# Optimization experiments

Hardware: AMD Instinct MI355X
Metric: run time of the kernel (lower is better)

Reference implementation:

```python
import jax, jax.numpy as jnp
import numpy as np

N_CLASSES = 1000
N_CENTERS = 4
SIGMA = 10.0
HIDDEN = 512
BATCH = 512


def setup_inputs() -> dict:
    key = jax.random.key(0)
    k1, k2 = jax.random.split(key)
    f = jax.random.normal(k1, (BATCH, HIDDEN), dtype=jnp.float32)
    # he_normal: std = sqrt(2 / fan_in), fan_in = hidden
    W = jax.random.normal(k2, (N_CLASSES, N_CENTERS, HIDDEN), dtype=jnp.float32) * np.sqrt(2.0 / HIDDEN)
    return {"f": f, "W": W}


def reference(f, W):
    n_classes, n_centers, hidden = W.shape
    mc = n_classes * n_centers
    w_flat = W.reshape(mc, hidden)  # [mc, h]

    # squared euclidean distance f<->centers via ||f||^2 + ||w||^2 - 2 f.w
    f_sq = jnp.sum(f * f, axis=-1, keepdims=True)            # [b, 1]
    w_sq = jnp.sum(w_flat * w_flat, axis=-1)                 # [mc]
    fw = jnp.einsum('bh,mh->bm', f, w_flat)                  # [b, mc]
    fw_norm = (f_sq + w_sq[None, :] - 2.0 * fw).reshape(f.shape[0], n_classes, n_centers)
    distance = jnp.max(jnp.exp(-fw_norm / SIGMA), axis=-1)   # [b, n_classes]

    # pairwise center distances, strict upper triangle regularizer
    ww = jnp.einsum('mh,nh->mn', w_flat, w_flat)             # [mc, mc]
    w_norm_mat = w_sq[:, None] + w_sq[None, :] - 2.0 * ww
    upper_mask = jnp.triu(jnp.ones((mc, mc), dtype=f.dtype), k=1)
    w_norm_upper = w_norm_mat * upper_mask
    denom = 2.0 / (mc * mc - mc)
    mu = denom * jnp.sum(w_norm_upper)
    residuals = ((w_norm_upper - mu) ** 2) * upper_mask
    rw = denom * jnp.sum(residuals)

    rw_col = jnp.full((f.shape[0], 1), rw, dtype=f.dtype) * jnp.ones((1, 1), dtype=f.dtype)
    rw_col = jnp.ones((f.shape[0], 1), dtype=f.dtype) * rw
    return jnp.concatenate([distance, rw_col], axis=-1)      # [b, n_classes+1]
```

## Files before the change

kernel.cpp:

```cpp
#include <hip/hip_runtime.h>


#define HIDDEN  512
#define BATCH   512
#define NCLASS  1000
#define MC      4000
#define MCPAD   4096
#define OUTW    1001
#define PAIRS   7998000.0

typedef __attribute__((ext_vector_type(8))) short bf16x8;
typedef __attribute__((ext_vector_type(4))) float f32x4;

static __device__ __forceinline__ unsigned short bfr(float x) {
  unsigned u = __float_as_uint(x);
  u += 0x7FFF + ((u >> 16) & 1);
  return (unsigned short)(u >> 16);
}
static __device__ __forceinline__ unsigned int pack2bf(float a, float b) {
  unsigned ua = __float_as_uint(a); ua += 0x7FFF + ((ua >> 16) & 1);
  unsigned ub = __float_as_uint(b); ub += 0x7FFF + ((ub >> 16) & 1);
  return (ua >> 16) | (ub & 0xFFFF0000u);
}

template <int STEPS>
static __device__ __forceinline__ void gemm22(
    const unsigned short* __restrict__ aP0, const unsigned short* __restrict__ aP1,
    const unsigned short* __restrict__ bP0, const unsigned short* __restrict__ bP1,
    f32x4 acc[2][2]) {
  bf16x8 aC[2], bC[2];
  aC[0] = *(const bf16x8*)aP0; aC[1] = *(const bf16x8*)aP1;
  bC[0] = *(const bf16x8*)bP0; bC[1] = *(const bf16x8*)bP1;
  #pragma unroll
  for (int kb = 0; kb < STEPS; kb++) {
    bf16x8 aN[2], bN[2];
    if (kb < STEPS - 1) {
      int off = (kb + 1) * 32;
      aN[0] = *(const bf16x8*)(aP0 + off); aN[1] = *(const bf16x8*)(aP1 + off);
      bN[0] = *(const bf16x8*)(bP0 + off); bN[1] = *(const bf16x8*)(bP1 + off);
    }
    #pragma unroll
    for (int mi = 0; mi < 2; mi++)
      #pragma unroll
      for (int ni = 0; ni < 2; ni++)
        acc[mi][ni] = __builtin_amdgcn_mfma_f32_16x16x32_bf16(aC[mi], bC[ni], acc[mi][ni], 0, 0, 0);
    if (kb < STEPS - 1) {
      aC[0] = aN[0]; aC[1] = aN[1]; bC[0] = bN[0]; bC[1] = bN[1];
    }
  }
}

__global__ __launch_bounds__(256) void prep_all_kernel(
    const float* __restrict__ f, const float* __restrict__ w,
    unsigned short* __restrict__ w2, unsigned short* __restrict__ f2,
    unsigned short* __restrict__ wt,
    float* __restrict__ w_sq, float* __restrict__ f_sq,
    float* __restrict__ s) {
  int bid = blockIdx.x;
  int t = threadIdx.x;
  if (bid < 1152) {
    if (bid == 0) { s[t] = 0.0f; s[t + 256] = 0.0f; }
    int lane = t & 63, wid = t >> 6;
    int row = bid * 4 + wid;
    const float* src = nullptr;
    unsigned short* dst2;
    float* dstsq;
    bool pad = false;
    if (row < MCPAD) {
      if (row < MC) src = w + (size_t)row * HIDDEN; else pad = true;
      dst2 = w2 + (size_t)row * HIDDEN; dstsq = w_sq + row;
    } else {
      int fr = row - MCPAD;
      src = f + (size_t)fr * HIDDEN;
      dst2 = f2 + (size_t)fr * HIDDEN; dstsq = f_sq + fr;
    }
    float4 a = {0.f,0.f,0.f,0.f}, b = {0.f,0.f,0.f,0.f};
    if (!pad) {
      const float4* s4 = (const float4*)src;
      a = s4[2 * lane]; b = s4[2 * lane + 1];
    }
    float sq = a.x*a.x + a.y*a.y + a.z*a.z + a.w*a.w
             + b.x*b.x + b.y*b.y + b.z*b.z + b.w*b.w;
    #pragma unroll
    for (int off = 32; off >= 1; off >>= 1) sq += __shfl_down(sq, off);
    if (lane == 0) *dstsq = sq;
    uint4 p;
    p.x = pack2bf(a.x, a.y); p.y = pack2bf(a.z, a.w);
    p.z = pack2bf(b.x, b.y); p.w = pack2bf(b.z, b.w);
    ((uint4*)dst2)[lane] = p;
  } else {
    int b2 = bid - 1152;
    int kb = b2 >> 3, ab = b2 & 7;
    __shared__ unsigned short tile[64][72];
    int c4 = (t & 15) * 4, r0 = t >> 4;
    #pragma unroll
    for (int i = 0; i < 4; i++) {
      int r = r0 + i * 16;
      int gk = kb * 64 + r;
      float4 v = {0.f,0.f,0.f,0.f};
      if (gk < MC) v = *(const float4*)&w[(size_t)gk * HIDDEN + ab * 64 + c4];
      tile[c4 + 0][r] = bfr(v.x);
      tile[c4 + 1][r] = bfr(v.y);
      tile[c4 + 2][r] = bfr(v.z);
      tile[c4 + 3][r] = bfr(v.w);
    }
    __syncthreads();
    #pragma unroll
    for (int i = 0; i < 4; i++) {
      int a = r0 + i * 16;
      uint2 v = *(const uint2*)&tile[a][c4];
      *(uint2*)&wt[(size_t)(ab * 64 + a) * MCPAD + kb * 64 + c4] = v;
    }
  }
}

__global__ __launch_bounds__(256) void colsum_kernel(
    const float* __restrict__ w, float* __restrict__ s) {
  int c = threadIdx.x * 2;
  int r0 = blockIdx.x * 125;
  float a0 = 0.f, a1 = 0.f;
  #pragma unroll 5
  for (int r = 0; r < 125; r++) {
    float2 v = *(const float2*)&w[(size_t)(r0 + r) * HIDDEN + c];
    a0 += v.x; a1 += v.y;
  }
  atomicAdd(&s[c], a0);
  atomicAdd(&s[c + 1], a1);
}

__global__ __launch_bounds__(256, 2) void main_kernel(
    const float* __restrict__ wOrig,
    const unsigned short* __restrict__ f2, const unsigned short* __restrict__ w2,
    const unsigned short* __restrict__ wt,
    const float* __restrict__ w_sq, const float* __restrict__ f_sq,
    const float* __restrict__ s,
    float* __restrict__ Gpart, float* __restrict__ rPart,
    float* __restrict__ out) {
  int bid = blockIdx.x;
  int t = threadIdx.x;
  int lane = t & 63, wid = t >> 6;
  int quad = lane >> 4, l16 = lane & 15;
  int waveM = (wid & 1) * 32, waveN = (wid >> 1) * 32;

  if (bid < 256) {
    int kc = bid >> 6, tIdx = bid & 63;
    int ta = tIdx >> 3, tb = tIdx & 7;
    size_t kBase = (size_t)kc * 1024;
    const unsigned short* aP0 = wt + (size_t)(ta * 64 + waveM + l16) * MCPAD + kBase + quad * 8;
    const unsigned short* aP1 = aP0 + (size_t)16 * MCPAD;
    const unsigned short* bP0 = wt + (size_t)(tb * 64 + waveN + l16) * MCPAD + kBase + quad * 8;
    const unsigned short* bP1 = bP0 + (size_t)16 * MCPAD;
    f32x4 acc[2][2] = {};
    gemm22<32>(aP0, aP1, bP0, bP1, acc);
    float* dst = Gpart + (size_t)kc * 262144 + (size_t)tIdx * 4096;
    #pragma unroll
    for (int mi = 0; mi < 2; mi++)
      #pragma unroll
      for (int ni = 0; ni < 2; ni++)
        #pragma unroll
        for (int r = 0; r < 4; r++) {
          int row = waveM + mi * 16 + quad * 4 + r;
          int col = waveN + ni * 16 + l16;
          dst[row * 64 + col] = acc[mi][ni][r];
        }
  } else if (bid < 768) {
    int idx = bid - 256;
    int rowBase = (idx >> 6) * 64, colBase = (idx & 63) * 64;
    const unsigned short* aP0 = f2 + (size_t)(rowBase + waveM + l16) * HIDDEN + quad * 8;
    const unsigned short* aP1 = aP0 + (size_t)16 * HIDDEN;
    const unsigned short* bP0 = w2 + (size_t)(colBase + waveN + l16) * HIDDEN + quad * 8;
    const unsigned short* bP1 = bP0 + (size_t)16 * HIDDEN;
    f32x4 acc[2][2] = {};
    gemm22<16>(aP0, aP1, bP0, bP1, acc);
    #pragma unroll
    for (int mi = 0; mi < 2; mi++)
      #pragma unroll
      for (int r = 0; r < 4; r++) {
        int grow = rowBase + waveM + mi * 16 + quad * 4 + r;
        float fs = f_sq[grow];
        #pragma unroll
        for (int ni = 0; ni < 2; ni++) {
          int gcol = colBase + waveN + ni * 16 + l16;
          float d = fs + w_sq[gcol] - 2.0f * acc[mi][ni][r];
          float e = __expf(-d * 0.1f);
          e = fmaxf(e, __shfl_xor(e, 1));
          e = fmaxf(e, __shfl_xor(e, 2));
          int cls = gcol >> 2;
          if ((l16 & 3) == 0 && cls < NCLASS)
            out[(size_t)grow * OUTW + cls] = e;
        }
      }
  } else {
    int row = (bid - 768) * 4 + wid;
    const float4* wr = (const float4*)&wOrig[(size_t)row * HIDDEN];
    const float4* s4 = (const float4*)s;
    float4 w0 = wr[2 * lane], w1 = wr[2 * lane + 1];
    float4 s0 = s4[2 * lane], s1 = s4[2 * lane + 1];
    float d = w0.x*s0.x + w0.y*s0.y + w0.z*s0.z + w0.w*s0.w
            + w1.x*s1.x + w1.y*s1.y + w1.z*s1.z + w1.w*s1.w;
    #pragma unroll
    for (int off = 32; off >= 1; off >>= 1) d += __shfl_down(d, off);
    if (lane == 0) rPart[row] = d;
  }
}

__global__ __launch_bounds__(256) void reduceF_kernel(
    const float* __restrict__ Gpart, float* __restrict__ fPart) {
  int t = threadIdx.x;
  int lane = t & 63, wid = t >> 6;
  size_t e = (size_t)blockIdx.x * 1024 + t * 4;
  float4 g0 = *(const float4*)&Gpart[e];
  float4 g1 = *(const float4*)&Gpart[e + 262144];
  float4 g2 = *(const float4*)&Gpart[e + 2 * 262144];
  float4 g3 = *(const float4*)&Gpart[e + 3 * 262144];
  float gx = g0.x + g1.x + g2.x + g3.x;
  float gy = g0.y + g1.y + g2.y + g3.y;
  float gz = g0.z + g1.z + g2.z + g3.z;
  float gw = g0.w + g1.w + g2.w + g3.w;
  float sum = gx * gx + gy * gy + gz * gz + gw * gw;
  #pragma unroll
  for (int off = 32; off >= 1; off >>= 1) sum += __shfl_down(sum, off);
  __shared__ float red[4];
  if (lane == 0) red[wid] = sum;
  __syncthreads();
  if (t == 0) fPart[blockIdx.x] = red[0] + red[1] + red[2] + red[3];
}

__global__ __launch_bounds__(512) void finalize_kernel(
    const float* __restrict__ w_sq, const float* __restrict__ rPart,
    const float* __restrict__ s, const float* __restrict__ fPart,
    float* __restrict__ out) {
  int t = threadIdx.x;
  int lane = t & 63, wid = t >> 6;
  float lT = 0.f, lQ = 0.f, lR = 0.f, lS, lF = 0.f;
  #pragma unroll
  for (int i = t; i < MCPAD; i += 512) {
    float q = w_sq[i];
    lT += q; lQ += q * q;
    if (i < MC) lR += q * rPart[i];
  }
  lS = s[t] * s[t];
  if (t < 256) lF = fPart[t];
  #pragma unroll
  for (int off = 32; off >= 1; off >>= 1) {
    lT += __shfl_down(lT, off); lQ += __shfl_down(lQ, off);
    lR += __shfl_down(lR, off); lS += __shfl_down(lS, off);
    lF += __shfl_down(lF, off);
  }
  __shared__ float red[8][5];
  __shared__ float rwS;
  if (lane == 0) {
    red[wid][0] = lT; red[wid][1] = lQ; red[wid][2] = lR;
    red[wid][3] = lS; red[wid][4] = lF;
  }
  __syncthreads();
  if (t == 0) {
    double T = 0, Q = 0, R = 0, Ssq = 0, F = 0;
    for (int i = 0; i < 8; i++) {
      T += red[i][0]; Q += red[i][1]; R += red[i][2];
      Ssq += red[i][3]; F += red[i][4];
    }
    double S1 = 4000.0 * T - Ssq;
    double S2 = 4000.0 * Q + T * T - 4.0 * R + 2.0 * F;
    double mu = S1 / PAIRS;
    rwS = (float)(S2 / PAIRS - mu * mu);
  }
  __syncthreads();
  out[(size_t)t * OUTW + NCLASS] = rwS;
}

extern "C" void kernel_launch(void* const* d_in, const int* in_sizes, int n_in,
                              void* d_out, int out_size, void* d_ws, size_t ws_size,
                              hipStream_t stream) {
  const float* f = (const float*)d_in[0];
  const float* w = (const float*)d_in[1];
  float* out = (float*)d_out;

  char* ws = (char*)d_ws;
  unsigned short* w2 = (unsigned short*)(ws);
  unsigned short* f2 = (unsigned short*)(ws + 4194304);
  unsigned short* wt = (unsigned short*)(ws + 4718592);
  float* Gpart = (float*)(ws + 8912896);
  float* w_sq  = (float*)(ws + 13107200);
  float* f_sq  = (float*)(ws + 13123584);
  float* s     = (float*)(ws + 13125632);
  float* rPart = (float*)(ws + 13127680);
  float* fPart = (float*)(ws + 13144064);

  prep_all_kernel<<<1664, 256, 0, stream>>>(f, w, w2, f2, wt, w_sq, f_sq, s);
  colsum_kernel<<<32, 256, 0, stream>>>(w, s);
  main_kernel<<<1768, 256, 0, stream>>>(w, f2, w2, wt, w_sq, f_sq, s, Gpart, rPart, out);
  reduceF_kernel<<<256, 256, 0, stream>>>(Gpart, fPart);
  finalize_kernel<<<1, 512, 0, stream>>>(w_sq, rPart, s, fPart, out);
}
```

Measured before the change: 115.1 us.

## Fuse regularizer reductions into main kernel with 128x128 tiles and atomic accumulation

The launch sequence drops from five kernels to three. The colsum, rPart and reduceF stages are folded into the main kernel. The Gram matrix W^T W is now computed whole over K by 16 blocks with 4x4 MFMA tiles per wave, and its Frobenius norm is reduced in-register and combined through an atomic, so the split-K partial buffer is never written or read back. Column sums s and the w_sq-weighted column sums v come from bf16 w2 rows, and sum(q*r) is rewritten algebraically as s·v. The distance GEMM uses larger 128x128 block tiles with double-buffered register loads. The trade-offs are far fewer blocks (208) with long serial K loops of 128 steps on 16 blocks, higher register pressure, float atomic ordering nondeterminism, and s/v built from bf16-rounded weights.

```diff
diff --git a/kernel.cpp b/kernel.cpp
--- a/kernel.cpp
+++ b/kernel.cpp
@@ -24,42 +24,52 @@
 }
 
 template <int STEPS>
-static __device__ __forceinline__ void gemm22(
-    const unsigned short* __restrict__ aP0, const unsigned short* __restrict__ aP1,
-    const unsigned short* __restrict__ bP0, const unsigned short* __restrict__ bP1,
-    f32x4 acc[2][2]) {
-  bf16x8 aC[2], bC[2];
-  aC[0] = *(const bf16x8*)aP0; aC[1] = *(const bf16x8*)aP1;
-  bC[0] = *(const bf16x8*)bP0; bC[1] = *(const bf16x8*)bP1;
+static __device__ __forceinline__ void gemm44(
+    const unsigned short* __restrict__ aBase, int ldA,
+    const unsigned short* __restrict__ bBase, int ldB,
+    f32x4 acc[4][4]) {
+  bf16x8 aB[2][4], bB[2][4];
+  #pragma unroll
+  for (int i = 0; i < 4; i++) {
+    aB[0][i] = *(const bf16x8*)(aBase + (size_t)(i * 16) * ldA);
+    bB[0][i] = *(const bf16x8*)(bBase + (size_t)(i * 16) * ldB);
+    aB[1][i] = *(const bf16x8*)(aBase + (size_t)(i * 16) * ldA + 32);
+    bB[1][i] = *(const bf16x8*)(bBase + (size_t)(i * 16) * ldB + 32);
+  }
   #pragma unroll
   for (int kb = 0; kb < STEPS; kb++) {
-    bf16x8 aN[2], bN[2];
-    if (kb < STEPS - 1) {
-      int off = (kb + 1) * 32;
-      aN[0] = *(const bf16x8*)(aP0 + off); aN[1] = *(const bf16x8*)(aP1 + off);
-      bN[0] = *(const bf16x8*)(bP0 + off); bN[1] = *(const bf16x8*)(bP1 + off);
-    }
-    #pragma unroll
-    for (int mi = 0; mi < 2; mi++)
-      #pragma unroll
-      for (int ni = 0; ni < 2; ni++)
-        acc[mi][ni] = __builtin_amdgcn_mfma_f32_16x16x32_bf16(aC[mi], bC[ni], acc[mi][ni], 0, 0, 0);
-    if (kb < STEPS - 1) {
-      aC[0] = aN[0]; aC[1] = aN[1]; bC[0] = bN[0]; bC[1] = bN[1];
-    }
-  }
-}
-
-__global__ __launch_bounds__(256) void prep_all_kernel(
+    int cur = kb & 1;
+    #pragma unroll
+    for (int mi = 0; mi < 4; mi++)
+      #pragma unroll
+      for (int ni = 0; ni < 4; ni++)
+        acc[mi][ni] = __builtin_amdgcn_mfma_f32_16x16x32_bf16(
+            aB[cur][mi], bB[cur][ni], acc[mi][ni], 0, 0, 0);
+    if (kb + 2 < STEPS) {
+      int off = (kb + 2) * 32;
+      #pragma unroll
+      for (int i = 0; i < 4; i++) {
+        aB[cur][i] = *(const bf16x8*)(aBase + (size_t)(i * 16) * ldA + off);
+        bB[cur][i] = *(const bf16x8*)(bBase + (size_t)(i * 16) * ldB + off);
+      }
+    }
+  }
+}
+
+__global__ __launch_bounds__(256) void prep_kernel(
     const float* __restrict__ f, const float* __restrict__ w,
     unsigned short* __restrict__ w2, unsigned short* __restrict__ f2,
     unsigned short* __restrict__ wt,
     float* __restrict__ w_sq, float* __restrict__ f_sq,
-    float* __restrict__ s) {
+    float* __restrict__ s, float* __restrict__ v, float* __restrict__ fAcc) {
   int bid = blockIdx.x;
   int t = threadIdx.x;
   if (bid < 1152) {
-    if (bid == 0) { s[t] = 0.0f; s[t + 256] = 0.0f; }
+    if (bid == 0) {
+      s[t] = 0.0f; s[t + 256] = 0.0f;
+      v[t] = 0.0f; v[t + 256] = 0.0f;
+      if (t == 0) fAcc[0] = 0.0f;
+    }
     int lane = t & 63, wid = t >> 6;
     int row = bid * 4 + wid;
     const float* src = nullptr;
@@ -97,90 +107,88 @@
     for (int i = 0; i < 4; i++) {
       int r = r0 + i * 16;
       int gk = kb * 64 + r;
-      float4 v = {0.f,0.f,0.f,0.f};
-      if (gk < MC) v = *(const float4*)&w[(size_t)gk * HIDDEN + ab * 64 + c4];
-      tile[c4 + 0][r] = bfr(v.x);
-      tile[c4 + 1][r] = bfr(v.y);
-      tile[c4 + 2][r] = bfr(v.z);
-      tile[c4 + 3][r] = bfr(v.w);
+      float4 vv = {0.f,0.f,0.f,0.f};
+      if (gk < MC) vv = *(const float4*)&w[(size_t)gk * HIDDEN + ab * 64 + c4];
+      tile[c4 + 0][r] = bfr(vv.x);
+      tile[c4 + 1][r] = bfr(vv.y);
+      tile[c4 + 2][r] = bfr(vv.z);
+      tile[c4 + 3][r] = bfr(vv.w);
     }
     __syncthreads();
     #pragma unroll
     for (int i = 0; i < 4; i++) {
       int a = r0 + i * 16;
-      uint2 v = *(const uint2*)&tile[a][c4];
-      *(uint2*)&wt[(size_t)(ab * 64 + a) * MCPAD + kb * 64 + c4] = v;
-    }
-  }
-}
-
-__global__ __launch_bounds__(256) void colsum_kernel(
-    const float* __restrict__ w, float* __restrict__ s) {
-  int c = threadIdx.x * 2;
-  int r0 = blockIdx.x * 125;
-  float a0 = 0.f, a1 = 0.f;
-  #pragma unroll 5
-  for (int r = 0; r < 125; r++) {
-    float2 v = *(const float2*)&w[(size_t)(r0 + r) * HIDDEN + c];
-    a0 += v.x; a1 += v.y;
-  }
-  atomicAdd(&s[c], a0);
-  atomicAdd(&s[c + 1], a1);
-}
-
-__global__ __launch_bounds__(256, 2) void main_kernel(
-    const float* __restrict__ wOrig,
+      uint2 vv = *(const uint2*)&tile[a][c4];
+      *(uint2*)&wt[(size_t)(ab * 64 + a) * MCPAD + kb * 64 + c4] = vv;
+    }
+  }
+}
+
+__global__ __launch_bounds__(256) void main_kernel(
     const unsigned short* __restrict__ f2, const unsigned short* __restrict__ w2,
     const unsigned short* __restrict__ wt,
     const float* __restrict__ w_sq, const float* __restrict__ f_sq,
-    const float* __restrict__ s,
-    float* __restrict__ Gpart, float* __restrict__ rPart,
+    float* __restrict__ s, float* __restrict__ v, float* __restrict__ fAcc,
     float* __restrict__ out) {
   int bid = blockIdx.x;
   int t = threadIdx.x;
   int lane = t & 63, wid = t >> 6;
   int quad = lane >> 4, l16 = lane & 15;
-  int waveM = (wid & 1) * 32, waveN = (wid >> 1) * 32;
-
-  if (bid < 256) {
-    int kc = bid >> 6, tIdx = bid & 63;
-    int ta = tIdx >> 3, tb = tIdx & 7;
-    size_t kBase = (size_t)kc * 1024;
-    const unsigned short* aP0 = wt + (size_t)(ta * 64 + waveM + l16) * MCPAD + kBase + quad * 8;
-    const unsigned short* aP1 = aP0 + (size_t)16 * MCPAD;
-    const unsigned short* bP0 = wt + (size_t)(tb * 64 + waveN + l16) * MCPAD + kBase + quad * 8;
-    const unsigned short* bP1 = bP0 + (size_t)16 * MCPAD;
-    f32x4 acc[2][2] = {};
-    gemm22<32>(aP0, aP1, bP0, bP1, acc);
-    float* dst = Gpart + (size_t)kc * 262144 + (size_t)tIdx * 4096;
-    #pragma unroll
-    for (int mi = 0; mi < 2; mi++)
-      #pragma unroll
-      for (int ni = 0; ni < 2; ni++)
+
+  if (bid < 16) {
+    int tm = bid >> 2, tn = bid & 3;
+    const unsigned short* aP =
+        wt + (size_t)(tm * 128 + (wid & 1) * 64 + l16) * MCPAD + quad * 8;
+    const unsigned short* bP =
+        wt + (size_t)(tn * 128 + (wid >> 1) * 64 + l16) * MCPAD + quad * 8;
+    f32x4 acc[4][4] = {};
+    gemm44<128>(aP, MCPAD, bP, MCPAD, acc);
+    float ff = 0.0f;
+    #pragma unroll
+    for (int mi = 0; mi < 4; mi++)
+      #pragma unroll
+      for (int ni = 0; ni < 4; ni++)
         #pragma unroll
-        for (int r = 0; r < 4; r++) {
-          int row = waveM + mi * 16 + quad * 4 + r;
-          int col = waveN + ni * 16 + l16;
-          dst[row * 64 + col] = acc[mi][ni][r];
-        }
-  } else if (bid < 768) {
-    int idx = bid - 256;
-    int rowBase = (idx >> 6) * 64, colBase = (idx & 63) * 64;
-    const unsigned short* aP0 = f2 + (size_t)(rowBase + waveM + l16) * HIDDEN + quad * 8;
-    const unsigned short* aP1 = aP0 + (size_t)16 * HIDDEN;
-    const unsigned short* bP0 = w2 + (size_t)(colBase + waveN + l16) * HIDDEN + quad * 8;
-    const unsigned short* bP1 = bP0 + (size_t)16 * HIDDEN;
-    f32x4 acc[2][2] = {};
-    gemm22<16>(aP0, aP1, bP0, bP1, acc);
-    #pragma unroll
-    for (int mi = 0; mi < 2; mi++)
+        for (int r = 0; r < 4; r++)
+          ff += acc[mi][ni][r] * acc[mi][ni][r];
+    #pragma unroll
+    for (int off = 32; off >= 1; off >>= 1) ff += __shfl_down(ff, off);
+    __shared__ float red[4];
+    if (lane == 0) red[wid] = ff;
+    __syncthreads();
+    if (t == 0) atomicAdd(&fAcc[0], red[0] + red[1] + red[2] + red[3]);
+  } else if (bid < 80) {
+    int r0 = (bid - 16) * 64;
+    int c = t * 2;
+    float s0 = 0.f, s1 = 0.f, v0 = 0.f, v1 = 0.f;
+    for (int r = 0; r < 64; r++) {
+      float q = w_sq[r0 + r];
+      unsigned u = *(const unsigned*)&w2[(size_t)(r0 + r) * HIDDEN + c];
+      float wa = __uint_as_float(u << 16);
+      float wb = __uint_as_float(u & 0xFFFF0000u);
+      s0 += wa; s1 += wb;
+      v0 += q * wa; v1 += q * wb;
+    }
+    atomicAdd(&s[c], s0); atomicAdd(&s[c + 1], s1);
+    atomicAdd(&v[c], v0); atomicAdd(&v[c + 1], v1);
+  } else {
+    int idx = bid - 80;
+    int rowBase = (idx >> 5) * 128, colBase = (idx & 31) * 128;
+    const unsigned short* aP =
+        f2 + (size_t)(rowBase + (wid & 1) * 64 + l16) * HIDDEN + quad * 8;
+    const unsigned short* bP =
+        w2 + (size_t)(colBase + (wid >> 1) * 64 + l16) * HIDDEN + quad * 8;
+    f32x4 acc[4][4] = {};
+    gemm44<16>(aP, HIDDEN, bP, HIDDEN, acc);
+    #pragma unroll
+    for (int mi = 0; mi < 4; mi++)
       #pragma unroll
       for (int r = 0; r < 4; r++) {
-        int grow = rowBase + waveM + mi * 16 + quad * 4 + r;
+        int grow = rowBase + (wid & 1) * 64 + mi * 16 + quad * 4 + r;
         float fs = f_sq[grow];
         #pragma unroll
-        for (int ni = 0; ni < 2; ni++) {
-          int gcol = colBase + waveN + ni * 16 + l16;
+        for (int ni = 0; ni < 4; ni++) {
+          int gcol = colBase + (wid >> 1) * 64 + ni * 16 + l16;
           float d = fs + w_sq[gcol] - 2.0f * acc[mi][ni][r];
           float e = __expf(-d * 0.1f);
           e = fmaxf(e, __shfl_xor(e, 1));
@@ -190,57 +198,24 @@
             out[(size_t)grow * OUTW + cls] = e;
         }
       }
-  } else {
-    int row = (bid - 768) * 4 + wid;
-    const float4* wr = (const float4*)&wOrig[(size_t)row * HIDDEN];
-    const float4* s4 = (const float4*)s;
-    float4 w0 = wr[2 * lane], w1 = wr[2 * lane + 1];
-    float4 s0 = s4[2 * lane], s1 = s4[2 * lane + 1];
-    float d = w0.x*s0.x + w0.y*s0.y + w0.z*s0.z + w0.w*s0.w
-            + w1.x*s1.x + w1.y*s1.y + w1.z*s1.z + w1.w*s1.w;
-    #pragma unroll
-    for (int off = 32; off >= 1; off >>= 1) d += __shfl_down(d, off);
-    if (lane == 0) rPart[row] = d;
-  }
-}
-
-__global__ __launch_bounds__(256) void reduceF_kernel(
-    const float* __restrict__ Gpart, float* __restrict__ fPart) {
-  int t = threadIdx.x;
-  int lane = t & 63, wid = t >> 6;
-  size_t e = (size_t)blockIdx.x * 1024 + t * 4;
-  float4 g0 = *(const float4*)&Gpart[e];
-  float4 g1 = *(const float4*)&Gpart[e + 262144];
-  float4 g2 = *(const float4*)&Gpart[e + 2 * 262144];
-  float4 g3 = *(const float4*)&Gpart[e + 3 * 262144];
-  float gx = g0.x + g1.x + g2.x + g3.x;
-  float gy = g0.y + g1.y + g2.y + g3.y;
-  float gz = g0.z + g1.z + g2.z + g3.z;
-  float gw = g0.w + g1.w + g2.w + g3.w;
-  float sum = gx * gx + gy * gy + gz * gz + gw * gw;
-  #pragma unroll
-  for (int off = 32; off >= 1; off >>= 1) sum += __shfl_down(sum, off);
-  __shared__ float red[4];
-  if (lane == 0) red[wid] = sum;
-  __syncthreads();
-  if (t == 0) fPart[blockIdx.x] = red[0] + red[1] + red[2] + red[3];
+  }
 }
 
 __global__ __launch_bounds__(512) void finalize_kernel(
-    const float* __restrict__ w_sq, const float* __restrict__ rPart,
-    const float* __restrict__ s, const float* __restrict__ fPart,
+    const float* __restrict__ w_sq, const float* __restrict__ s,
+    const float* __restrict__ v, const float* __restrict__ fAcc,
     float* __restrict__ out) {
   int t = threadIdx.x;
   int lane = t & 63, wid = t >> 6;
-  float lT = 0.f, lQ = 0.f, lR = 0.f, lS, lF = 0.f;
+  float lT = 0.f, lQ = 0.f;
   #pragma unroll
   for (int i = t; i < MCPAD; i += 512) {
     float q = w_sq[i];
     lT += q; lQ += q * q;
-    if (i < MC) lR += q * rPart[i];
-  }
-  lS = s[t] * s[t];
-  if (t < 256) lF = fPart[t];
+  }
+  float lR = s[t] * v[t];
+  float lS = s[t] * s[t];
+  float lF = (t == 0) ? fAcc[0] : 0.0f;
   #pragma unroll
   for (int off = 32; off >= 1; off >>= 1) {
     lT += __shfl_down(lT, off); lQ += __shfl_down(lQ, off);
@@ -280,16 +255,13 @@
   unsigned short* w2 = (unsigned short*)(ws);
   unsigned short* f2 = (unsigned short*)(ws + 4194304);
   unsigned short* wt = (unsigned short*)(ws + 4718592);
-  float* Gpart = (float*)(ws + 8912896);
-  float* w_sq  = (float*)(ws + 13107200);
-  float* f_sq  = (float*)(ws + 13123584);
-  float* s     = (float*)(ws + 13125632);
-  float* rPart = (float*)(ws + 13127680);
-  float* fPart = (float*)(ws + 13144064);
-
-  prep_all_kernel<<<1664, 256, 0, stream>>>(f, w, w2, f2, wt, w_sq, f_sq, s);
-  colsum_kernel<<<32, 256, 0, stream>>>(w, s);
-  main_kernel<<<1768, 256, 0, stream>>>(w, f2, w2, wt, w_sq, f_sq, s, Gpart, rPart, out);
-  reduceF_kernel<<<256, 256, 0, stream>>>(Gpart, fPart);
-  finalize_kernel<<<1, 512, 0, stream>>>(w_sq, rPart, s, fPart, out);
-}
+  float* w_sq  = (float*)(ws + 8912896);
+  float* f_sq  = (float*)(ws + 8929280);
+  float* s     = (float*)(ws + 8931328);
+  float* v     = (float*)(ws + 8933376);
+  float* fAcc  = (float*)(ws + 8935424);
+
+  prep_kernel<<<1664, 256, 0, stream>>>(f, w, w2, f2, wt, w_sq, f_sq, s, v, fAcc);
+  main_kernel<<<208, 256, 0, stream>>>(f2, w2, wt, w_sq, f_sq, s, v, fAcc, out);
+  finalize_kernel<<<1, 512, 0, stream>>>(w_sq, s, v, fAcc, out);
+}
```

New measurement: 183.4 us. 1.59x slower.
